# Kernel tuning notes

Measured on AMD Instinct MI355X. Metric: run time of the kernel, lower is better.

## Reference

```python
import jax, jax.numpy as jnp
import numpy as np

IN, H, C = 128, 512, 32
B, T = 64, 512


def _gru_cell(x, h, W_ih, W_hh, b_ih, b_hh):
    # PyTorch GRUCell: gates ordered (r, z, n)
    gi = x @ W_ih.T + b_ih          # [B, 3H]
    gh = h @ W_hh.T + b_hh          # [B, 3H]
    i_r, i_z, i_n = jnp.split(gi, 3, axis=-1)
    h_r, h_z, h_n = jnp.split(gh, 3, axis=-1)
    r = jax.nn.sigmoid(i_r + h_r)
    z = jax.nn.sigmoid(i_z + h_z)
    n = jnp.tanh(i_n + r * h_n)
    return (1.0 - z) * n + z * h


def setup_inputs() -> dict:
    key = jax.random.key(0)
    ks = jax.random.split(key, 20)
    d = {
        "x": jax.random.normal(ks[0], (B, T, IN), dtype=jnp.float32),
        "h0_1": 0.1 * jax.random.normal(ks[1], (B, H), dtype=jnp.float32),
        "h0_2": 0.1 * jax.random.normal(ks[2], (B, H), dtype=jnp.float32),
        "h0_3": 0.1 * jax.random.normal(ks[3], (B, H), dtype=jnp.float32),
    }
    ins = [IN, H, H]
    i = 4
    for l in range(3):
        s_in = 1.0 / np.sqrt(ins[l])
        d[f"W_ih{l+1}"] = s_in * jax.random.normal(ks[i], (3 * H, ins[l]), dtype=jnp.float32); i += 1
        d[f"W_hh{l+1}"] = (1.0 / np.sqrt(H)) * jax.random.normal(ks[i], (3 * H, H), dtype=jnp.float32); i += 1
        d[f"b_ih{l+1}"] = jnp.zeros((3 * H,), dtype=jnp.float32)
        d[f"b_hh{l+1}"] = jnp.zeros((3 * H,), dtype=jnp.float32)
    d["W_out"] = (1.0 / np.sqrt(H)) * jax.random.normal(ks[i], (C, H), dtype=jnp.float32); i += 1
    d["b_out"] = jax.random.uniform(ks[i], (C,), dtype=jnp.float32)
    return d


def reference(x, h0_1, h0_2, h0_3,
              W_ih1, W_hh1, b_ih1, b_hh1,
              W_ih2, W_hh2, b_ih2, b_hh2,
              W_ih3, W_hh3, b_ih3, b_hh3,
              W_out, b_out):
    xT = jnp.transpose(x, (1, 0, 2))  # [T, B, IN]

    def step(carry, xt):
        h1, h2, h3 = carry
        h1 = _gru_cell(xt, h1, W_ih1, W_hh1, b_ih1, b_hh1)
        h2 = _gru_cell(h1, h2, W_ih2, W_hh2, b_ih2, b_hh2)
        h3 = _gru_cell(h2, h3, W_ih3, W_hh3, b_ih3, b_hh3)
        y = jax.nn.softmax(h3 @ W_out.T + b_out, axis=1)  # [B, C]
        return (h1, h2, h3), y

    _, Y = jax.lax.scan(step, (h0_1, h0_2, h0_3), xT)  # Y: [T, B, C]
    return jnp.transpose(Y, (1, 0, 2))  # [B, T, C]
```

## Files before the change

kernel.cpp:

```cpp
#include <hip/hip_runtime.h>

typedef unsigned short u16;
typedef unsigned int u32;
typedef unsigned long long u64;
typedef __attribute__((ext_vector_type(8))) short bf16x8;
typedef __attribute__((ext_vector_type(4))) float f32x4;

#define T_ 512
#define B_ 64
#define IN_ 128
#define H_ 512
#define C_ 32
#define BH_ (B_ * H_)
#define NWG_CELL 192
#define NWG_TOT 196

#define FA(L, mb)       ((((L) * 4 + (mb))) * 32)
#define FG(L, mb)       (((12 + (L) * 4 + (mb))) * 32)
#define FRA(Lm, mb, s)  (((24 + ((Lm) * 4 + (mb)) * 3 + (s))) * 32)
#define FRG(Lm, mb, s)  (((48 + ((Lm) * 4 + (mb)) * 3 + (s))) * 32)
#define FO(mb, s)       (((72 + (mb) * 3 + (s))) * 32)
#define NFLAG 84

#define DEVINL __device__ __attribute__((always_inline)) inline

DEVINL u16 f2bf_(float f) {
    u32 u = __float_as_uint(f);
    u32 r = (u + 0x7FFFu + ((u >> 16) & 1u)) >> 16;
    return (u16)r;
}
DEVINL float bf2f_(u16 h) { return __uint_as_float(((u32)h) << 16); }

DEVINL u64 ld_llc_u64(const u64* p) {
    return __hip_atomic_load((u64*)p, __ATOMIC_RELAXED, __HIP_MEMORY_SCOPE_AGENT);
}
DEVINL void st_llc_u32(u32* p, u32 v) {
    __hip_atomic_store(p, v, __ATOMIC_RELAXED, __HIP_MEMORY_SCOPE_AGENT);
}
DEVINL u32 ld_flag(const u32* p) {
    return __hip_atomic_load((u32*)p, __ATOMIC_RELAXED, __HIP_MEMORY_SCOPE_AGENT);
}
DEVINL u32 add_flag(u32* p) {
    return __hip_atomic_fetch_add(p, 1u, __ATOMIC_RELAXED, __HIP_MEMORY_SCOPE_AGENT);
}
DEVINL void st_flag(u32* p, u32 v) {
    __hip_atomic_store(p, v, __ATOMIC_RELAXED, __HIP_MEMORY_SCOPE_AGENT);
}
DEVINL void wait_ge(u32* p, u32 v) {
    while (ld_flag(p) < v) __builtin_amdgcn_s_sleep(1);
}

__global__ void split_kernel(const float* __restrict__ src, u16* __restrict__ hi,
                             u16* __restrict__ lo, int n) {
    int i = blockIdx.x * 256 + threadIdx.x;
    if (i < n) {
        float f = src[i];
        u16 h = f2bf_(f);
        hi[i] = h;
        lo[i] = f2bf_(f - bf2f_(h));
    }
}

struct Params {
    const float* x;
    const u16* ih_hi[3]; const u16* ih_lo[3];
    const u16* hh_hi[3]; const u16* hh_lo[3];
    const float* b_ih[3]; const float* b_hh[3];
    const u16* wout_hi; const u16* wout_lo;
    const float* b_out;
    u16* h_hi; u16* h_lo;
    u32* bar;
    float* y;
};

DEVINL bf16x8 ld8(const u16* p) { return *reinterpret_cast<const bf16x8*>(p); }

DEVINL bf16x8 ld8_lds(const u16* s, int row, int kb) {
    const int bo = (row << 10) + (((kb) << 1) ^ ((row & 7) << 4));
    return *reinterpret_cast<const bf16x8*>((const char*)s + bo);
}

DEVINL f32x4 mfma3(bf16x8 ah, bf16x8 al, bf16x8 bh, bf16x8 bl, f32x4 c) {
    c = __builtin_amdgcn_mfma_f32_16x16x32_bf16(ah, bh, c, 0, 0, 0);
    c = __builtin_amdgcn_mfma_f32_16x16x32_bf16(al, bh, c, 0, 0, 0);
    c = __builtin_amdgcn_mfma_f32_16x16x32_bf16(ah, bl, c, 0, 0, 0);
    return c;
}

DEVINL void gemm3_reg(const u16* sAh, const u16* sAl, int row,
                      const bf16x8 (&w)[3][2][16], int lhi,
                      f32x4& o0, f32x4& o1, f32x4& o2) {
    f32x4 a0 = {0.f,0.f,0.f,0.f}, a1 = {0.f,0.f,0.f,0.f}, a2 = {0.f,0.f,0.f,0.f};
#pragma unroll
    for (int kt = 0; kt < 16; ++kt) {
        const int kb = kt * 32 + lhi * 8;
        bf16x8 ah = ld8_lds(sAh, row, kb), al = ld8_lds(sAl, row, kb);
        a0 = mfma3(ah, al, w[0][0][kt], w[0][1][kt], a0);
        a1 = mfma3(ah, al, w[1][0][kt], w[1][1][kt], a1);
        a2 = mfma3(ah, al, w[2][0][kt], w[2][1][kt], a2);
    }
    o0 = a0; o1 = a1; o2 = a2;
}

DEVINL void gemm2_reg(const u16* sAh, const u16* sAl, int row,
                      const bf16x8 (&w)[3][2][16], int lhi,
                      f32x4& o0, f32x4& o1) {
    f32x4 a0 = {0.f,0.f,0.f,0.f}, a1 = {0.f,0.f,0.f,0.f};
#pragma unroll
    for (int kt = 0; kt < 16; ++kt) {
        const int kb = kt * 32 + lhi * 8;
        bf16x8 ah = ld8_lds(sAh, row, kb), al = ld8_lds(sAl, row, kb);
        a0 = mfma3(ah, al, w[0][0][kt], w[0][1][kt], a0);
        a1 = mfma3(ah, al, w[1][0][kt], w[1][1][kt], a1);
    }
    o0 = a0; o1 = a1;
}

DEVINL void stage_h(const u16* ghi, const u16* glo,
                    u16* shi, u16* slo, int b0, int tid) {
#pragma unroll
    for (int c = 0; c < 2; ++c) {
        u64 rh[4], rl[4];
#pragma unroll
        for (int k = 0; k < 4; ++k) {
            const int idx = tid + ((c * 4 + k) << 8);
            const int row = idx >> 7, col = idx & 127;
            rh[k] = ld_llc_u64((const u64*)(ghi + (size_t)(b0 + row) * H_) + col);
            rl[k] = ld_llc_u64((const u64*)(glo + (size_t)(b0 + row) * H_) + col);
        }
#pragma unroll
        for (int k = 0; k < 4; ++k) {
            const int idx = tid + ((c * 4 + k) << 8);
            const int row = idx >> 7;
            const int so = (row << 10) + (((idx & 127) << 3) ^ ((row & 7) << 4));
            *(u64*)((char*)shi + so) = rh[k];
            *(u64*)((char*)slo + so) = rl[k];
        }
    }
}

DEVINL void store_sg(float (&dst)[16][33], f32x4 a, int col, int lhi) {
#pragma unroll
    for (int q = 0; q < 4; ++q) dst[lhi * 4 + q][col] = a[q];
}

__global__ __launch_bounds__(256, 1) void gru_pipe(Params p) {
    __shared__ u16 hs[4][8192];
    __shared__ float sg[6][16][33];
    __shared__ float slog[16][33];
    const int wg = blockIdx.x, tid = threadIdx.x;
    const int wave = tid >> 6, lane = tid & 63;
    const int ln15 = lane & 15, lhi = lane >> 4;
    u32* F = p.bar;

    bf16x8 wreg[3][2][16];
    const int L = (wg < NWG_CELL) ? (wg >> 6) : 0;
    const int wgl = wg & 63, ug = wgl & 15, mb = wgl >> 4;
    const int u0 = ug * 32, b0c = mb * 16;
    const int tt0 = wave * 3;
    if (wg < NWG_CELL) {
        if (wave >= 2) {
#pragma unroll
            for (int j = 0; j < 3; ++j) {
                const int tt = tt0 + j, g = (tt >> 1) - 3, c = (tt & 1) * 16 + ln15;
                const u16* bh = p.hh_hi[L] + (size_t)(g * H_ + u0 + c) * H_;
                const u16* bl = p.hh_lo[L] + (size_t)(g * H_ + u0 + c) * H_;
#pragma unroll
                for (int kt = 0; kt < 16; ++kt) {
                    wreg[j][0][kt] = ld8(bh + kt * 32 + lhi * 8);
                    wreg[j][1][kt] = ld8(bl + kt * 32 + lhi * 8);
                }
            }
        } else if (L > 0) {
#pragma unroll
            for (int j = 0; j < 3; ++j) {
                const int tt = tt0 + j, g = tt >> 1, c = (tt & 1) * 16 + ln15;
                const u16* bh = p.ih_hi[L] + (size_t)(g * H_ + u0 + c) * H_;
                const u16* bl = p.ih_lo[L] + (size_t)(g * H_ + u0 + c) * H_;
#pragma unroll
                for (int kt = 0; kt < 16; ++kt) {
                    wreg[j][0][kt] = ld8(bh + kt * 32 + lhi * 8);
                    wreg[j][1][kt] = ld8(bl + kt * 32 + lhi * 8);
                }
            }
        } else {
#pragma unroll
            for (int j = 0; j < 3; ++j) {
                const int tt = tt0 + j, g = tt >> 1, c = (tt & 1) * 16 + ln15;
                const u16* bh = p.ih_hi[0] + (size_t)(g * H_ + u0 + c) * IN_;
                const u16* bl = p.ih_lo[0] + (size_t)(g * H_ + u0 + c) * IN_;
#pragma unroll
                for (int kt = 0; kt < 4; ++kt) {
                    wreg[j][0][kt] = ld8(bh + kt * 32 + lhi * 8);
                    wreg[j][1][kt] = ld8(bl + kt * 32 + lhi * 8);
                }
            }
        }
    } else if (wave == 0) {
#pragma unroll
        for (int j = 0; j < 2; ++j) {
            const u16* bh = p.wout_hi + (size_t)(j * 16 + ln15) * H_;
            const u16* bl = p.wout_lo + (size_t)(j * 16 + ln15) * H_;
#pragma unroll
            for (int kt = 0; kt < 16; ++kt) {
                wreg[j][0][kt] = ld8(bh + kt * 32 + lhi * 8);
                wreg[j][1][kt] = ld8(bl + kt * 32 + lhi * 8);
            }
        }
    }

    if (wg < NWG_CELL) {
        for (int t = 0; t < T_; ++t) {
            const int sCur = t % 3, sPrev = (t + 2) % 3;
            if (tid == 0) {
                u32* gO = &F[FG(L, mb)];
                const u32 thrO = (u32)t;
                u32* gI = (L > 0) ? &F[FG(L - 1, mb)] : gO;
                const u32 thrI = (L > 0) ? (u32)(t + 1) : 0u;
                u32* gW = gO; u32 thrW = 0u;
                if (t >= 3) {
                    thrW = (u32)((t - 3) / 3) + 1u;
                    gW = (L < 2) ? &F[FRG(L, mb, sCur)] : &F[FO(mb, sCur)];
                }
                while ((u32)(ld_flag(gO) < thrO) | (u32)(ld_flag(gI) < thrI) |
                       (u32)(ld_flag(gW) < thrW)) {
                    __builtin_amdgcn_s_sleep(1);
                }
            }
            __syncthreads();

            stage_h(p.h_hi + (size_t)(3 * L + sPrev) * BH_,
                    p.h_lo + (size_t)(3 * L + sPrev) * BH_, hs[0], hs[1], b0c, tid);
            if (L > 0)
                stage_h(p.h_hi + (size_t)(3 * (L - 1) + sCur) * BH_,
                        p.h_lo + (size_t)(3 * (L - 1) + sCur) * BH_, hs[2], hs[3], b0c, tid);
            __syncthreads();
            if (tid == 0 && L > 0) {
                const u32 k = (u32)(t / 3) + 1u;
                u32 old = add_flag(&F[FRA(L - 1, mb, sCur)]);
                if (old == 16u * k - 1u) st_flag(&F[FRG(L - 1, mb, sCur)], k);
            }

            f32x4 oA, oB, oC;
            if (wave < 2 && L == 0) {
                const float* xr = p.x + (size_t)(b0c + ln15) * (T_ * IN_) + (size_t)t * IN_;
                f32x4 a0 = {0.f,0.f,0.f,0.f}, a1 = {0.f,0.f,0.f,0.f}, a2 = {0.f,0.f,0.f,0.f};
#pragma unroll
                for (int kt = 0; kt < 4; ++kt) {
                    const int kb = kt * 32 + lhi * 8;
                    bf16x8 ah, al;
#pragma unroll
                    for (int j = 0; j < 8; ++j) {
                        float f = xr[kb + j];
                        u16 hb = f2bf_(f);
                        ah[j] = (short)hb;
                        al[j] = (short)f2bf_(f - bf2f_(hb));
                    }
                    a0 = mfma3(ah, al, wreg[0][0][kt], wreg[0][1][kt], a0);
                    a1 = mfma3(ah, al, wreg[1][0][kt], wreg[1][1][kt], a1);
                    a2 = mfma3(ah, al, wreg[2][0][kt], wreg[2][1][kt], a2);
                }
                oA = a0; oB = a1; oC = a2;
            } else {
                const u16* sAh = (wave < 2) ? hs[2] : hs[0];
                const u16* sAl = (wave < 2) ? hs[3] : hs[1];
                gemm3_reg(sAh, sAl, ln15, wreg, lhi, oA, oB, oC);
            }
            {
                const int gA = (tt0    ) >> 1, cA = ((tt0    ) & 1) * 16 + ln15;
                const int gB = (tt0 + 1) >> 1, cB = ((tt0 + 1) & 1) * 16 + ln15;
                const int gC = (tt0 + 2) >> 1, cC = ((tt0 + 2) & 1) * 16 + ln15;
                store_sg(sg[gA], oA, cA, lhi);
                store_sg(sg[gB], oB, cB, lhi);
                store_sg(sg[gC], oC, cC, lhi);
            }
            __syncthreads();

            {
                const int rb = tid & 15, uu = tid >> 4;
                const int colu = uu * 2;
                const int gcol = u0 + colu;
                const u32 hp2h = *(const u32*)((const char*)hs[0] + (rb << 10) + ((gcol * 2) ^ ((rb & 7) << 4)));
                const u32 hp2l = *(const u32*)((const char*)hs[1] + (rb << 10) + ((gcol * 2) ^ ((rb & 7) << 4)));
                u32 packh = 0, packl = 0;
#pragma unroll
                for (int half = 0; half < 2; ++half) {
                    const int uc = colu + half;
                    const int uidx = u0 + uc;
                    const float ir  = sg[0][rb][uc] + p.b_ih[L][uidx];
                    const float iz  = sg[1][rb][uc] + p.b_ih[L][H_ + uidx];
                    const float in_ = sg[2][rb][uc] + p.b_ih[L][2 * H_ + uidx];
                    const float hr  = sg[3][rb][uc] + p.b_hh[L][uidx];
                    const float hz  = sg[4][rb][uc] + p.b_hh[L][H_ + uidx];
                    const float hn  = sg[5][rb][uc] + p.b_hh[L][2 * H_ + uidx];
                    const float r = 1.f / (1.f + expf(-(ir + hr)));
                    const float z = 1.f / (1.f + expf(-(iz + hz)));
                    const float n = tanhf(in_ + r * hn);
                    const float hprev = bf2f_((u16)((half ? (hp2h >> 16) : hp2h) & 0xffffu))
                                      + bf2f_((u16)((half ? (hp2l >> 16) : hp2l) & 0xffffu));
                    const float hnew = (1.f - z) * n + z * hprev;
                    const u16 nh = f2bf_(hnew);
                    const u16 nl = f2bf_(hnew - bf2f_(nh));
                    packh |= (u32)nh << (16 * half);
                    packl |= (u32)nl << (16 * half);
                }
                u16* ho_hi = p.h_hi + (size_t)(3 * L + sCur) * BH_;
                u16* ho_lo = p.h_lo + (size_t)(3 * L + sCur) * BH_;
                const size_t hx = (size_t)(b0c + rb) * H_ + gcol;
                st_llc_u32((u32*)(ho_hi + hx), packh);
                st_llc_u32((u32*)(ho_lo + hx), packl);
            }
            __syncthreads();
            if (tid == 0) {
                u32 old = add_flag(&F[FA(L, mb)]);
                if (old == 16u * (u32)(t + 1) - 1u) st_flag(&F[FG(L, mb)], (u32)(t + 1));
            }
        }
    } else {
        const int mbo = wg - NWG_CELL, b0 = mbo * 16;
        for (int t = 0; t < T_; ++t) {
            const int s = t % 3;
            if (tid == 0) wait_ge(&F[FG(2, mbo)], (u32)(t + 1));
            __syncthreads();
            stage_h(p.h_hi + (size_t)(6 + s) * BH_, p.h_lo + (size_t)(6 + s) * BH_,
                    hs[0], hs[1], b0, tid);
            __syncthreads();
            if (tid == 0) add_flag(&F[FO(mbo, s)]);
            if (wave == 0) {
                f32x4 a0, a1;
                gemm2_reg(hs[0], hs[1], ln15, wreg, lhi, a0, a1);
#pragma unroll
                for (int q = 0; q < 4; ++q) {
                    slog[lhi * 4 + q][ln15] = a0[q];
                    slog[lhi * 4 + q][16 + ln15] = a1[q];
                }
            }
            __syncthreads();
            if (tid < 16) {
                float v[32];
                float m = -1e30f;
#pragma unroll
                for (int c = 0; c < 32; ++c) { v[c] = slog[tid][c] + p.b_out[c]; m = fmaxf(m, v[c]); }
                float sden = 0.f;
#pragma unroll
                for (int c = 0; c < 32; ++c) { v[c] = expf(v[c] - m); sden += v[c]; }
                const float inv = 1.f / sden;
                float* yp = p.y + ((size_t)(b0 + tid) * T_ + t) * C_;
#pragma unroll
                for (int c = 0; c < 32; ++c) yp[c] = v[c] * inv;
            }
        }
    }
}

extern "C" void kernel_launch(void* const* d_in, const int* in_sizes, int n_in,
                              void* d_out, int out_size, void* d_ws, size_t ws_size,
                              hipStream_t stream) {
    (void)in_sizes; (void)n_in; (void)out_size; (void)ws_size;

    const float* x      = (const float*)d_in[0];
    const float* h0[3]  = {(const float*)d_in[1], (const float*)d_in[2], (const float*)d_in[3]};
    const float* Wih[3] = {(const float*)d_in[4], (const float*)d_in[8], (const float*)d_in[12]};
    const float* Whh[3] = {(const float*)d_in[5], (const float*)d_in[9], (const float*)d_in[13]};
    const float* bih[3] = {(const float*)d_in[6], (const float*)d_in[10], (const float*)d_in[14]};
    const float* bhh[3] = {(const float*)d_in[7], (const float*)d_in[11], (const float*)d_in[15]};
    const float* Wout   = (const float*)d_in[16];
    const float* bout   = (const float*)d_in[17];

    u16* w = (u16*)d_ws;
    size_t off = 0;
    auto take = [&](size_t n) { u16* p = w + off; off += n; return p; };
    u16 *ihh[3], *ihl[3], *hhh[3], *hhl[3];
    const size_t szih[3] = {(size_t)3 * H_ * IN_, (size_t)3 * H_ * H_, (size_t)3 * H_ * H_};
    const size_t szhh = (size_t)3 * H_ * H_;
    for (int l = 0; l < 3; ++l) {
        ihh[l] = take(szih[l]); ihl[l] = take(szih[l]);
        hhh[l] = take(szhh);    hhl[l] = take(szhh);
    }
    u16* wouth = take((size_t)C_ * H_);
    u16* woutl = take((size_t)C_ * H_);
    u16* hhi = take((size_t)3 * 3 * BH_);
    u16* hlo = take((size_t)3 * 3 * BH_);
    off = (off + 255) & ~(size_t)255;
    u32* bar = (u32*)take(2 * (NFLAG * 32));
    const size_t bar_bytes = (size_t)NFLAG * 32 * sizeof(u32);

    hipMemsetAsync(bar, 0, bar_bytes, stream);

    auto split = [&](const float* src, u16* hi, u16* lo, int n) {
        split_kernel<<<dim3((n + 255) / 256), dim3(256), 0, stream>>>(src, hi, lo, n);
    };
    for (int l = 0; l < 3; ++l) {
        split(Wih[l], ihh[l], ihl[l], (int)szih[l]);
        split(Whh[l], hhh[l], hhl[l], (int)szhh);
    }
    split(Wout, wouth, woutl, C_ * H_);
    for (int l = 0; l < 3; ++l)
        split(h0[l], hhi + (size_t)(3 * l + 2) * BH_, hlo + (size_t)(3 * l + 2) * BH_, BH_);

    Params p;
    p.x = x;
    for (int l = 0; l < 3; ++l) {
        p.ih_hi[l] = ihh[l]; p.ih_lo[l] = ihl[l];
        p.hh_hi[l] = hhh[l]; p.hh_lo[l] = hhl[l];
        p.b_ih[l] = bih[l];  p.b_hh[l] = bhh[l];
    }
    p.wout_hi = wouth; p.wout_lo = woutl; p.b_out = bout;
    p.h_hi = hhi; p.h_lo = hlo;
    p.bar = bar;
    p.y = (float*)d_out;

    void* args[] = {&p};
    hipError_t err = hipLaunchCooperativeKernel((void*)gru_pipe, dim3(NWG_TOT), dim3(256),
                                                args, 0u, stream);
    if (err != hipSuccess) {
        gru_pipe<<<dim3(NWG_TOT), dim3(256), 0, stream>>>(p);
    }
}
```

Before: 3.030 ms.

## Prefetch lower-layer input state and x ahead of the recurrent wait

Moves staging of the previous layer's hidden state for step t+1 to the end of step t, so it is fetched before the same-layer dependency wait, and loads layer-0 input x into registers before the flag spin. The flag increment moves to a different thread so the signal is not serialized behind the next wait. This aims to take input-side loads off the per-timestep recurrent critical path. It adds an extra barrier per step and changes when the ring-buffer slot is read relative to release flags, which could affect correctness of the 3-slot reuse protocol.

```diff
diff --git a/kernel.cpp b/kernel.cpp
--- a/kernel.cpp
+++ b/kernel.cpp
@@ -210,30 +210,37 @@
     }
 
     if (wg < NWG_CELL) {
+        if (L > 0) {
+            if (tid == 0) wait_ge(&F[FG(L - 1, mb)], 1u);
+            __syncthreads();
+            stage_h(p.h_hi + (size_t)(3 * (L - 1)) * BH_,
+                    p.h_lo + (size_t)(3 * (L - 1)) * BH_, hs[2], hs[3], b0c, tid);
+        }
         for (int t = 0; t < T_; ++t) {
             const int sCur = t % 3, sPrev = (t + 2) % 3;
+
+            float xq[32];
+            if (L == 0 && wave < 2) {
+                const float* xr = p.x + (size_t)(b0c + ln15) * (T_ * IN_) + (size_t)t * IN_;
+#pragma unroll
+                for (int kt = 0; kt < 4; ++kt)
+#pragma unroll
+                    for (int j = 0; j < 8; ++j)
+                        xq[kt * 8 + j] = xr[kt * 32 + lhi * 8 + j];
+            }
+
             if (tid == 0) {
                 u32* gO = &F[FG(L, mb)];
                 const u32 thrO = (u32)t;
-                u32* gI = (L > 0) ? &F[FG(L - 1, mb)] : gO;
-                const u32 thrI = (L > 0) ? (u32)(t + 1) : 0u;
                 u32* gW = gO; u32 thrW = 0u;
                 if (t >= 3) {
                     thrW = (u32)((t - 3) / 3) + 1u;
                     gW = (L < 2) ? &F[FRG(L, mb, sCur)] : &F[FO(mb, sCur)];
                 }
-                while ((u32)(ld_flag(gO) < thrO) | (u32)(ld_flag(gI) < thrI) |
-                       (u32)(ld_flag(gW) < thrW)) {
+                while ((u32)(ld_flag(gO) < thrO) | (u32)(ld_flag(gW) < thrW)) {
                     __builtin_amdgcn_s_sleep(1);
                 }
             }
-            __syncthreads();
-
-            stage_h(p.h_hi + (size_t)(3 * L + sPrev) * BH_,
-                    p.h_lo + (size_t)(3 * L + sPrev) * BH_, hs[0], hs[1], b0c, tid);
-            if (L > 0)
-                stage_h(p.h_hi + (size_t)(3 * (L - 1) + sCur) * BH_,
-                        p.h_lo + (size_t)(3 * (L - 1) + sCur) * BH_, hs[2], hs[3], b0c, tid);
             __syncthreads();
             if (tid == 0 && L > 0) {
                 const u32 k = (u32)(t / 3) + 1u;
@@ -241,17 +248,19 @@
                 if (old == 16u * k - 1u) st_flag(&F[FRG(L - 1, mb, sCur)], k);
             }
 
+            stage_h(p.h_hi + (size_t)(3 * L + sPrev) * BH_,
+                    p.h_lo + (size_t)(3 * L + sPrev) * BH_, hs[0], hs[1], b0c, tid);
+            __syncthreads();
+
             f32x4 oA, oB, oC;
             if (wave < 2 && L == 0) {
-                const float* xr = p.x + (size_t)(b0c + ln15) * (T_ * IN_) + (size_t)t * IN_;
                 f32x4 a0 = {0.f,0.f,0.f,0.f}, a1 = {0.f,0.f,0.f,0.f}, a2 = {0.f,0.f,0.f,0.f};
 #pragma unroll
                 for (int kt = 0; kt < 4; ++kt) {
-                    const int kb = kt * 32 + lhi * 8;
                     bf16x8 ah, al;
 #pragma unroll
                     for (int j = 0; j < 8; ++j) {
-                        float f = xr[kb + j];
+                        float f = xq[kt * 8 + j];
                         u16 hb = f2bf_(f);
                         ah[j] = (short)hb;
                         al[j] = (short)f2bf_(f - bf2f_(hb));
@@ -311,9 +320,16 @@
                 st_llc_u32((u32*)(ho_lo + hx), packl);
             }
             __syncthreads();
-            if (tid == 0) {
+            if (tid == 64) {
                 u32 old = add_flag(&F[FA(L, mb)]);
                 if (old == 16u * (u32)(t + 1) - 1u) st_flag(&F[FG(L, mb)], (u32)(t + 1));
+            }
+            if (L > 0 && t + 1 < T_) {
+                if (tid == 0) wait_ge(&F[FG(L - 1, mb)], (u32)(t + 2));
+                __syncthreads();
+                const int sNext = (t + 1) % 3;
+                stage_h(p.h_hi + (size_t)(3 * (L - 1) + sNext) * BH_,
+                        p.h_lo + (size_t)(3 * (L - 1) + sNext) * BH_, hs[2], hs[3], b0c, tid);
             }
         }
     } else {
```

Result: slower. 3.371 ms (+11.3%).
